# Performance work log

Measured on AMD Instinct MI355X. Metric: run time of the kernel, lower is better.

## Reference

```python
import jax, jax.numpy as jnp
import numpy as np
import math

B, L, C, Hh, Ww = 1, 16, 32, 64, 64
Wf = Ww // 2 + 1
R = 16
GROUPS = 4
MID = 4  # max(C//16, 4)
DT_REF = 1.0
INJ_K = 2.0
EPS = 1e-5


def _conv2d(x, w, b):
    y = jax.lax.conv_general_dilated(x, w, (1, 1), 'SAME',
                                     dimension_numbers=('NCHW', 'OIHW', 'NCHW'))
    return y + b[None, :, None, None]


def _adaptive_avg_w(x, out_w):
    # adaptive avg pool along last axis (torch AdaptiveAvgPool semantics)
    w_in = x.shape[-1]
    cs = jnp.concatenate([jnp.zeros(x.shape[:-1] + (1,), x.dtype), jnp.cumsum(x, -1)], -1)
    starts = np.floor(np.arange(out_w) * w_in / out_w).astype(np.int32)
    ends = np.ceil((np.arange(out_w) + 1) * w_in / out_w).astype(np.int32)
    num = cs[..., ends] - cs[..., starts]
    den = jnp.asarray(ends - starts, x.dtype)
    return num / den


def setup_inputs() -> dict:
    key = jax.random.key(0)
    ks = jax.random.split(key, 24)
    s = 0.05
    inp = {}
    inp['x'] = jax.random.normal(ks[0], (B, C, L, Hh, Ww), jnp.float32)
    inp['dt'] = jax.random.uniform(ks[1], (B, L), jnp.float32, 0.1, 1.0)
    inp['conv1_w'] = jax.random.normal(ks[2], (C, C, 3, 3), jnp.float32) * s
    inp['conv1_b'] = jnp.zeros((C,), jnp.float32)
    inp['conv2_w'] = jax.random.normal(ks[3], (C, C, 3, 3), jnp.float32) * s
    inp['conv2_b'] = jnp.zeros((C,), jnp.float32)
    inp['gfc_w'] = jax.random.normal(ks[4], (C, C), jnp.float32) * s
    inp['gfc_b'] = jnp.zeros((C,), jnp.float32)
    inp['head_w'] = jax.random.normal(ks[5], (C * R * 3, C), jnp.float32) * 0.02
    hb = np.zeros((C, R, 3), np.float32); hb[..., 0] = 1.0; hb[..., 2] = -5.0
    inp['head_b'] = jnp.asarray(hb.reshape(-1))
    inp['mix_w'] = jnp.eye(2 * R, dtype=jnp.float32) + jax.random.normal(ks[6], (2 * R, 2 * R), jnp.float32) * 0.02
    inp['mix_b'] = jnp.zeros((2 * R,), jnp.float32)
    inp['rank_scale'] = jnp.ones((R,), jnp.float32)
    inp['proj_w'] = jax.random.normal(ks[7], (1, R), jnp.float32) * s
    inp['proj_b'] = jnp.zeros((1,), jnp.float32)
    inp['pif_w'] = jax.random.normal(ks[8], (C, C), jnp.float32) * s  # 1x1x1 Conv3d
    inp['pif_b'] = jnp.zeros((C,), jnp.float32)
    inp['gn_w'] = jnp.ones((C,), jnp.float32)
    inp['gn_b'] = jnp.zeros((C,), jnp.float32)
    inp['g1_w'] = jax.random.normal(ks[9], (MID, C), jnp.float32) * s
    inp['g1_b'] = jnp.zeros((MID,), jnp.float32)
    inp['g2_w'] = jax.random.normal(ks[10], (C, MID), jnp.float32) * s
    inp['g2_b'] = jnp.zeros((C,), jnp.float32)
    return inp


def _forward(x, dt, conv1_w, conv1_b, conv2_w, conv2_b, gfc_w, gfc_b, head_w, head_b,
             mix_w, mix_b, rank_scale, proj_w, proj_b, pif_w, pif_b, gn_w, gn_b,
             g1_w, g1_b, g2_w, g2_b):
    Bx, Cx, Lx, H, W = x.shape
    x_seq = jnp.transpose(x, (0, 2, 1, 3, 4))  # [B,L,C,H,W]
    # ---- DynamicsParameterEstimator on flattened [B*L,C,H,W] ----
    xf = x_seq.reshape(Bx * Lx, Cx, H, W)
    f = jax.nn.silu(_conv2d(xf, conv1_w, conv1_b))
    f = jax.nn.silu(_conv2d(f, conv2_w, conv2_b))
    glob = jax.nn.sigmoid(f.mean((2, 3)) @ gfc_w.T + gfc_b)  # [BL,C]
    f = f * glob[:, :, None, None]
    f = _adaptive_avg_w(f.mean(2), Wf)         # [BL,C,Wf]
    feat = jnp.transpose(f, (0, 2, 1))          # [BL,Wf,C]
    p = (feat @ head_w.T + head_b).reshape(Bx * Lx, Wf, Cx, R, 3)
    nu = jax.nn.softplus(p[..., 0]).reshape(Bx, Lx, Wf, Cx, R)
    th = (jnp.tanh(p[..., 1]) * math.pi).reshape(Bx, Lx, Wf, Cx, R)
    sg = jax.nn.sigmoid(p[..., 2]).reshape(Bx, Lx, Wf, Cx, R)
    nu = jnp.transpose(nu, (0, 1, 3, 2, 4))[:, :, :, None]  # [B,L,C,1,Wf,R]
    th = jnp.transpose(th, (0, 1, 3, 2, 4))[:, :, :, None]
    sg = jnp.transpose(sg, (0, 1, 3, 2, 4))[:, :, :, None]
    # ---- Koopman A (triton kernel math): exp(-nu*dt) * exp(i*theta*dt) ----
    dtb = dt[:, :, None, None, None, None]
    decay = jnp.exp(-nu * dtb)
    ang = th * dtb
    A = jax.lax.complex(decay * jnp.cos(ang), decay * jnp.sin(ang))  # [B,L,C,1,Wf,R]
    # ---- injection in rfft space, gated by dt ----
    g = 1.0 - jnp.exp(-INJ_K * jnp.clip(dt / max(DT_REF, 1e-6), 0.0))  # [B,L]
    xfreq = jnp.fft.rfft(x_seq, axis=-1)        # [B,L,C,H,Wf] complex
    u = sg * xfreq[..., None] * g[:, :, None, None, None, None]  # [B,L,C,H,Wf,R]
    # ---- parallel linear recurrence h_t = A_t h_{t-1} + u_t ----
    def combine(a, b):
        Aa, ua = a
        Ab, ub = b
        return (Ab * Aa, Ab * ua + ub)
    _, h = jax.lax.associative_scan(combine, (A, u), axis=1)  # h: [B,L,C,H,Wf,R]
    # ---- SpectralMixer over rank (real/imag stacked) ----
    hs = jnp.concatenate([h.real, h.imag], -1) @ mix_w.T + mix_b
    hr, hi = jnp.split(hs, 2, -1)
    h = jax.lax.complex(hr, hi) * rank_scale
    # ---- rank projection + irfft ----
    y = jnp.einsum('blchfr,r->blchf', h, proj_w[0].astype(h.dtype)) + proj_b[0]
    y = jnp.fft.irfft(y, n=W, axis=-1)          # [B,L,C,H,W]
    y = jnp.transpose(y, (0, 2, 1, 3, 4))        # [B,C,L,H,W]
    # ---- post_ifft_proj: 1x1x1 Conv3d ----
    y = jnp.einsum('bclhw,oc->bolhw', y, pif_w) + pif_b[None, :, None, None, None]
    # ---- SpatialGroupNorm (per-frame GroupNorm, 4 groups) ----
    z = jnp.transpose(y, (0, 2, 1, 3, 4)).reshape(Bx * Lx, GROUPS, (Cx // GROUPS) * H * W)
    mu = z.mean(-1, keepdims=True)
    var = z.var(-1, keepdims=True)
    z = (z - mu) / jnp.sqrt(var + EPS)
    z = z.reshape(Bx, Lx, Cx, H, W) * gn_w[None, None, :, None, None] + gn_b[None, None, :, None, None]
    y = jnp.transpose(z, (0, 2, 1, 3, 4))        # [B,C,L,H,W]
    # ---- LatitudeGating (squeeze-excite over W) ----
    ym = y.mean(-1)                              # [B,C,L,H]
    yg = jnp.transpose(ym, (0, 2, 3, 1))          # [B,L,H,C]
    yg = jax.nn.sigmoid(jax.nn.silu(yg @ g1_w.T + g1_b) @ g2_w.T + g2_b)
    gate = jnp.transpose(yg, (0, 3, 1, 2))[..., None]  # [B,C,L,H,1]
    return x + y * gate


def reference(x, dt, conv1_w, conv1_b, conv2_w, conv2_b, gfc_w, gfc_b, head_w, head_b,
              mix_w, mix_b, rank_scale, proj_w, proj_b, pif_w, pif_b, gn_w, gn_b,
              g1_w, g1_b, g2_w, g2_b):
    return _forward(x, dt, conv1_w, conv1_b, conv2_w, conv2_b, gfc_w, gfc_b, head_w,
                    head_b, mix_w, mix_b, rank_scale, proj_w, proj_b, pif_w, pif_b,
                    gn_w, gn_b, g1_w, g1_b, g2_w, g2_b)
```

## Files before the change

### kernel.cpp

```cpp
#include <hip/hip_runtime.h>
#include <hip/hip_bf16.h>
#include <math.h>

#define CC 32
#define LL 16
#define HH 64
#define WW 64
#define WF 33
#define RR 16
#define PI_F 3.14159265358979323846f

typedef __attribute__((ext_vector_type(8))) short short8;
typedef __attribute__((ext_vector_type(4))) float f32x4;

#define OFF_F1      0
#define OFF_COLSUM  2097152
#define OFF_FEAT    2130944
#define OFF_ARE     2147840
#define OFF_AIM     2418176
#define OFF_SGG     2688512
#define OFF_XFR     2958848
#define OFF_XFI     4040192
#define OFF_YFR     5121536
#define OFF_YFI     6202880
#define OFF_PART    2958848
#define OFF_Y1      2958848
#define OFF_Y2      0
#define OFF_GNM     7284224
#define OFF_GNR     7284288
#define OFF_YM      7284352
#define OFF_GATE    7317120
#define OFF_WVEC    7349888
#define OFF_WT      7350016
#define OFF_YQ      7370496

__device__ __forceinline__ float sigmoidf_(float x){ return 1.0f/(1.0f+expf(-x)); }
__device__ __forceinline__ unsigned short f2bf(float v){
    __hip_bfloat16 b = __float2bfloat16(v);
    return *reinterpret_cast<unsigned short*>(&b);
}
__device__ __forceinline__ float bf2f(unsigned short u){
    __hip_bfloat16 b = *reinterpret_cast<__hip_bfloat16*>(&u);
    return __bfloat162float(b);
}

__global__ void k_prep0(const float* __restrict__ mix_w, const float* __restrict__ mix_b,
                        const float* __restrict__ rank_scale, const float* __restrict__ proj_w,
                        const float* __restrict__ proj_b,
                        const float* __restrict__ c1w, const float* __restrict__ c2w,
                        float* __restrict__ ws){
    unsigned short* wt = (unsigned short*)(ws + OFF_WT);
    if (blockIdx.x == 0){
        float* wv = ws + OFF_WVEC;
        int t = threadIdx.x;
        if (t < 32){
            float sre=0.f, sim=0.f;
            for (int r=0;r<RR;r++){
                float a = proj_w[r]*rank_scale[r];
                sre += a*mix_w[r*2*RR + t];
                sim += a*mix_w[(RR+r)*2*RR + t];
            }
            wv[t] = sre; wv[32+t] = sim;
        }
        if (t == 0){
            float cre=0.f, cim=0.f;
            for (int r=0;r<RR;r++){
                float a = proj_w[r]*rank_scale[r];
                cre += a*mix_b[r];
                cim += a*mix_b[RR+r];
            }
            wv[64] = cre + proj_b[0]; wv[65] = cim;
        }
        return;
    }
    int i = (blockIdx.x-1)*256 + threadIdx.x;
    if (i < 18432){
        int which = (i >= 9216);
        int j = which ? i - 9216 : i;
        int je   = j & 7;
        int lane = (j >> 3) & 63;
        int ct   = (j >> 9) & 1;
        int tap  = j >> 10;
        int kh = tap/3, kw = tap - kh*3;
        int co = ct*16 + (lane & 15);
        int ci = (lane >> 4)*8 + je;
        const float* cw = which ? c2w : c1w;
        wt[i] = f2bf(cw[((co*CC + ci)*3 + kh)*3 + kw]);
        return;
    }
    i -= 18432;
    if (i < 10240){
        int j = i & 7, lane = (i>>3)&63, cch = (i>>9)&3, t = i>>11;
        int frow = t*16 + (lane & 15);
        int k = ((lane>>4)&3)*8 + j;
        int w = (cch & 1)*32 + k;
        float coef = 0.f;
        if (frow < 33)       coef =  cosf(2.0f*PI_F*(float)(frow*w)/64.0f);
        else if (frow < 66)  coef = -sinf(2.0f*PI_F*(float)((frow-33)*w)/64.0f);
        unsigned short hi = f2bf(coef);
        wt[18432 + i] = (cch < 2) ? hi : f2bf(coef - bf2f(hi));
        return;
    }
    i -= 10240;
    if (i < 12288){
        int wtile = i / 3072;
        int rem = i - wtile*3072;
        int ch = rem >> 9;
        int ll = rem & 511;
        int lane = ll >> 3, j = ll & 7;
        int w = wtile*16 + (lane & 15);
        int k = (ch % 3)*32 + ((lane>>4)&3)*8 + j;
        float coef = 0.f;
        if (k < 33){
            float s = (k==0 || k==32) ? 1.f : 2.f;
            coef = s*cosf(2.0f*PI_F*(float)(k*w)/64.0f)*(1.0f/64.0f);
        } else if (k < 66){
            int f = k - 33;
            float s = (f==0 || f==32) ? 1.f : 2.f;
            coef = -s*sinf(2.0f*PI_F*(float)(f*w)/64.0f)*(1.0f/64.0f);
        }
        unsigned short hi = f2bf(coef);
        wt[18432 + 10240 + i] = (ch < 3) ? hi : f2bf(coef - bf2f(hi));
        return;
    }
}

__global__ __launch_bounds__(256, 4) void k_conv1m(const float* __restrict__ x,
                                                   const unsigned short* __restrict__ wt,
                                                   const float* __restrict__ cb,
                                                   unsigned short* __restrict__ f1p){
    __shared__ __align__(16) unsigned short xs[4*66*32];
    __shared__ __align__(16) unsigned short pw[9216];

    const int tid  = threadIdx.x;
    const int l    = blockIdx.x >> 5;
    const int h0   = (blockIdx.x & 31)*2;
    const int wid  = tid >> 6;
    const int lane = tid & 63;
    const int col  = lane & 15;
    const int kgrp = lane >> 4;

    {
        const unsigned int* src = (const unsigned int*)wt;
        unsigned int* dst = (unsigned int*)pw;
        #pragma unroll
        for (int j = 0; j < 18; ++j) dst[tid + j*256] = src[tid + j*256];
    }
    {
        const int rr = tid >> 6;
        const int w  = tid & 63;
        int hh = h0 - 1 + rr;
        bool hv = (hh >= 0 && hh < HH);
        const float* sp = x + (long)l*HH*WW + hh*WW + w;
        int wIdx = 1 + w;
        #pragma unroll
        for (int cib = 0; cib < 4; ++cib){
            float v[8];
            #pragma unroll
            for (int k = 0; k < 8; ++k)
                v[k] = hv ? sp[(long)(cib*8 + k)*LL*HH*WW] : 0.f;
            uint4 p;
            p.x = (unsigned)f2bf(v[0]) | ((unsigned)f2bf(v[1])<<16);
            p.y = (unsigned)f2bf(v[2]) | ((unsigned)f2bf(v[3])<<16);
            p.z = (unsigned)f2bf(v[4]) | ((unsigned)f2bf(v[5])<<16);
            p.w = (unsigned)f2bf(v[6]) | ((unsigned)f2bf(v[7])<<16);
            int cs = cib ^ (wIdx & 3);
            *(uint4*)&xs[(rr*66 + wIdx)*32 + cs*8] = p;
        }
    }
    if (tid < 32){
        int row = tid >> 3, rest = tid & 7;
        int wIdx = (rest >> 2) ? 65 : 0;
        int cib = rest & 3;
        *(uint4*)&xs[(row*66 + wIdx)*32 + cib*8] = make_uint4(0,0,0,0);
    }
    __syncthreads();

    #pragma unroll
    for (int u = 0; u < 4; ++u){
        int unit = wid + u*4;
        int hloc = unit >> 3;
        int rem  = unit & 7;
        int ct   = rem >> 2;
        int wt16 = rem & 3;
        int colw = wt16*16 + col;
        f32x4 acc = {0.f,0.f,0.f,0.f};
        #pragma unroll
        for (int kh = 0; kh < 3; ++kh){
            #pragma unroll
            for (int kw = 0; kw < 3; ++kw){
                int wIdx = colw + kw;
                int cs = kgrp ^ (wIdx & 3);
                short8 b = *(const short8*)&xs[((hloc+kh)*66 + wIdx)*32 + cs*8];
                short8 a = *(const short8*)&pw[((kh*3+kw)*2 + ct)*512 + lane*8];
                acc = __builtin_amdgcn_mfma_f32_16x16x32_bf16(a, b, acc, 0, 0, 0);
            }
        }
        int co0 = ct*16 + kgrp*4;
        int h = h0 + hloc;
        float o[4];
        #pragma unroll
        for (int r = 0; r < 4; ++r){
            float v = acc[r] + cb[co0+r];
            o[r] = v * sigmoidf_(v);
        }
        uint2 pk;
        pk.x = (unsigned)f2bf(o[0]) | ((unsigned)f2bf(o[1])<<16);
        pk.y = (unsigned)f2bf(o[2]) | ((unsigned)f2bf(o[3])<<16);
        *(uint2*)&f1p[(((long)l*HH + h)*WW + colw)*32 + co0] = pk;
    }
}

__global__ __launch_bounds__(256, 4) void k_conv2m(const unsigned short* __restrict__ f1p,
                                                   const unsigned short* __restrict__ wt,
                                                   const float* __restrict__ cb,
                                                   float* __restrict__ ws){
    __shared__ __align__(16) unsigned short xs[4*66*32];
    __shared__ __align__(16) unsigned short pw[9216];

    const int tid  = threadIdx.x;
    const int l    = blockIdx.x >> 5;
    const int h0   = (blockIdx.x & 31)*2;
    const int wid  = tid >> 6;
    const int lane = tid & 63;
    const int col  = lane & 15;
    const int kgrp = lane >> 4;

    {
        const unsigned int* src = (const unsigned int*)wt;
        unsigned int* dst = (unsigned int*)pw;
        #pragma unroll
        for (int j = 0; j < 18; ++j) dst[tid + j*256] = src[tid + j*256];
    }
    {
        const int rr = tid >> 6;
        const int w  = tid & 63;
        int hh = h0 - 1 + rr;
        bool hv = (hh >= 0 && hh < HH);
        const uint4* sp = (const uint4*)&f1p[(((long)l*HH + hh)*WW + w)*32];
        int wIdx = 1 + w;
        #pragma unroll
        for (int cib = 0; cib < 4; ++cib){
            uint4 p = hv ? sp[cib] : make_uint4(0,0,0,0);
            int cs = cib ^ (wIdx & 3);
            *(uint4*)&xs[(rr*66 + wIdx)*32 + cs*8] = p;
        }
    }
    if (tid < 32){
        int row = tid >> 3, rest = tid & 7;
        int wIdx = (rest >> 2) ? 65 : 0;
        int cib = rest & 3;
        *(uint4*)&xs[(row*66 + wIdx)*32 + cib*8] = make_uint4(0,0,0,0);
    }
    __syncthreads();

    #pragma unroll
    for (int u = 0; u < 4; ++u){
        int unit = wid + u*4;
        int hloc = unit >> 3;
        int rem  = unit & 7;
        int ct   = rem >> 2;
        int wt16 = rem & 3;
        int colw = wt16*16 + col;
        f32x4 acc = {0.f,0.f,0.f,0.f};
        #pragma unroll
        for (int kh = 0; kh < 3; ++kh){
            #pragma unroll
            for (int kw = 0; kw < 3; ++kw){
                int wIdx = colw + kw;
                int cs = kgrp ^ (wIdx & 3);
                short8 b = *(const short8*)&xs[((hloc+kh)*66 + wIdx)*32 + cs*8];
                short8 a = *(const short8*)&pw[((kh*3+kw)*2 + ct)*512 + lane*8];
                acc = __builtin_amdgcn_mfma_f32_16x16x32_bf16(a, b, acc, 0, 0, 0);
            }
        }
        int co0 = ct*16 + kgrp*4;
        int h = h0 + hloc;
        float* pp = ws + OFF_PART + ((long)(l*HH + h))*2048 + colw;
        #pragma unroll
        for (int r = 0; r < 4; ++r){
            float v = acc[r] + cb[co0+r];
            pp[(co0+r)*WW] = v * sigmoidf_(v);
        }
    }
}

__global__ void k_colred(float* __restrict__ ws){
    int b = blockIdx.x;
    int l = b >> 5, c = b & 31;
    int w = threadIdx.x;
    const float* p = ws + OFF_PART + (long)l*HH*2048 + c*WW + w;
    float s = 0.f;
    #pragma unroll 8
    for (int h = 0; h < HH; ++h) s += p[h*2048];
    ws[OFF_COLSUM + (l*CC + c)*WW + w] = s;
}

__global__ void k_globfeat(const float* __restrict__ gfc_w, const float* __restrict__ gfc_b,
                           float* __restrict__ ws){
    __shared__ float gs[CC], gl[CC];
    int l = blockIdx.x;
    int tid = threadIdx.x;
    if (tid < 32){
        const float* cs = ws + OFF_COLSUM + (l*CC+tid)*WW;
        float s = 0.f;
        for (int w=0;w<WW;w++) s += cs[w];
        gs[tid] = s;
    }
    __syncthreads();
    if (tid < 32){
        float acc = gfc_b[tid];
        for (int i=0;i<CC;i++) acc += gs[i]*(1.0f/4096.0f)*gfc_w[tid*CC+i];
        gl[tid] = sigmoidf_(acc);
    }
    __syncthreads();
    for (int i = tid; i < WF*CC; i += 256){
        int c = i & 31, wf = i >> 5;
        int s = (wf*64)/33;
        int e = ((wf+1)*64 + 32)/33;
        const float* cs = ws + OFF_COLSUM + (l*CC+c)*WW;
        float sum = 0.f;
        for (int w=s;w<e;w++) sum += cs[w];
        ws[OFF_FEAT + (l*WF+wf)*CC + c] = gl[c] * sum / (64.0f*(float)(e-s));
    }
}

__global__ void k_head(const float* __restrict__ hw, const float* __restrict__ hb,
                       const float* __restrict__ dt, float* __restrict__ ws){
    int t = blockIdx.x*blockDim.x + threadIdx.x;
    if (t >= LL*WF*CC*RR) return;
    int r = t & 15, c = (t>>4) & 31;
    int lw_ = t >> 9;
    int wf = lw_ % WF, l = lw_ / WF;
    const float* feat = ws + OFF_FEAT + (l*WF+wf)*CC;
    int j0 = (c*RR + r)*3;
    const float* w0 = hw + j0*CC;
    float p0=hb[j0], p1=hb[j0+1], p2=hb[j0+2];
    for (int i=0;i<CC;i++){
        float fv = feat[i];
        p0 += fv*w0[i]; p1 += fv*w0[CC+i]; p2 += fv*w0[2*CC+i];
    }
    float nu = fmaxf(p0,0.f) + log1pf(expf(-fabsf(p0)));
    float th = tanhf(p1)*PI_F;
    float sg = sigmoidf_(p2);
    float dtv = dt[l];
    float decay = expf(-nu*dtv);
    float ang = th*dtv;
    float g = 1.0f - expf(-2.0f*fmaxf(dtv,0.f));
    int idx = ((l*CC+c)*WF+wf)*RR + r;
    ws[OFF_ARE+idx] = decay*cosf(ang);
    ws[OFF_AIM+idx] = decay*sinf(ang);
    ws[OFF_SGG+idx] = sg*g;
}

__global__ __launch_bounds__(256, 4) void k_rfftm(const float* __restrict__ x,
                                                  const unsigned short* __restrict__ at,
                                                  float* __restrict__ ws){
    __shared__ __align__(16) unsigned short xs[HH*68];
    int b = blockIdx.x; int l = b >> 5, c = b & 31;
    int tid = threadIdx.x;
    const int wid  = tid >> 6;
    const int lane = tid & 63;
    const int col  = lane & 15;
    const int kgrp = lane >> 4;

    const float* xp = x + (long)(c*LL + l)*HH*WW;
    for (int i = tid; i < HH*WW; i += 256){
        int h = i >> 6, w = i & 63;
        xs[h*68 + w] = f2bf(xp[i]);
    }
    __syncthreads();

    float* xfr = ws + OFF_XFR + (long)(l*CC + c)*HH*WF;
    float* xfi = ws + OFF_XFI + (long)(l*CC + c)*HH*WF;
    #pragma unroll
    for (int q = 0; q < 5; ++q){
        int unit = wid + q*4;
        int ftile = unit >> 2;
        int htile = unit & 3;
        f32x4 acc = {0.f,0.f,0.f,0.f};
        #pragma unroll
        for (int cch = 0; cch < 4; ++cch){
            short8 a = *(const short8*)&at[(((ftile*4 + cch)*64) + lane)*8];
            short8 bb = *(const short8*)&xs[(htile*16 + col)*68 + (cch & 1)*32 + kgrp*8];
            acc = __builtin_amdgcn_mfma_f32_16x16x32_bf16(a, bb, acc, 0, 0, 0);
        }
        int h = htile*16 + col;
        #pragma unroll
        for (int r = 0; r < 4; ++r){
            int fr = ftile*16 + kgrp*4 + r;
            if (fr < 33)      xfr[fr*HH + h] = acc[r];
            else if (fr < 66) xfi[(fr-33)*HH + h] = acc[r];
        }
    }
}

__global__ __launch_bounds__(256) void k_scan(float* __restrict__ ws){
    __shared__ float lA[LL*RR], lI[LL*RR], lS[LL*RR];
    __shared__ float wv[66];
    int b = blockIdx.x;
    int c = b / WF, f = b - c*WF;
    int tid = threadIdx.x;
    if (tid < 66) wv[tid] = ws[OFF_WVEC + tid];
    {
        int l = tid >> 4, r = tid & 15;
        int src = ((l*CC + c)*WF + f)*RR + r;
        lA[tid] = ws[OFF_ARE + src];
        lI[tid] = ws[OFF_AIM + src];
        lS[tid] = ws[OFF_SGG + src];
    }
    __syncthreads();
    const int h  = tid >> 2;
    const int rq = tid & 3;
    float sre[4] = {0,0,0,0}, sim[4] = {0,0,0,0};
    float w0_[4], w1_[4], w2_[4], w3_[4];
    #pragma unroll
    for (int q=0;q<4;q++){
        int r = rq*4 + q;
        w0_[q]=wv[r]; w1_[q]=wv[16+r]; w2_[q]=wv[32+r]; w3_[q]=wv[48+r];
    }
    const float cre = wv[64], cim = wv[65];
    const long fh = (long)(c*WF + f)*HH + h;
    #pragma unroll 1
    for (int l=0;l<LL;l++){
        float xr = ws[OFF_XFR + l*(CC*HH*WF) + fh];
        float xi = ws[OFF_XFI + l*(CC*HH*WF) + fh];
        float yr = 0.f, yi = 0.f;
        #pragma unroll
        for (int q=0;q<4;q++){
            int r = rq*4 + q;
            float a = lA[l*16+r], ii = lI[l*16+r], s = lS[l*16+r];
            float nre = a*sre[q] - ii*sim[q] + s*xr;
            float nim = a*sim[q] + ii*sre[q] + s*xi;
            sre[q]=nre; sim[q]=nim;
            yr += w0_[q]*nre + w1_[q]*nim;
            yi += w2_[q]*nre + w3_[q]*nim;
        }
        yr += __shfl_xor(yr, 1); yr += __shfl_xor(yr, 2);
        yi += __shfl_xor(yi, 1); yi += __shfl_xor(yi, 2);
        if (rq == 0){
            ws[OFF_YFR + l*(CC*HH*WF) + fh] = yr + cre;
            ws[OFF_YFI + l*(CC*HH*WF) + fh] = yi + cim;
        }
    }
}

__global__ __launch_bounds__(256, 4) void k_irfftm(const unsigned short* __restrict__ btb,
                                                   float* __restrict__ ws){
    __shared__ __align__(16) unsigned short mh[HH*100];
    int b = blockIdx.x; int l = b >> 5, c = b & 31;
    int tid = threadIdx.x;
    const int wid  = tid >> 6;
    const int lane = tid & 63;
    const int col  = lane & 15;
    const int kgrp = lane >> 4;

    const float* Yr = ws + OFF_YFR + (long)(l*CC + c)*HH*WF;
    const float* Yi = ws + OFF_YFI + (long)(l*CC + c)*HH*WF;
    for (int i = tid; i < 33*64; i += 256){
        int f = i >> 6, h = i & 63;
        mh[h*100 + f]      = f2bf(Yr[i]);
        mh[h*100 + 33 + f] = f2bf(Yi[i]);
    }
    for (int i = tid; i < 64*34; i += 256){
        int h = i / 34, f = 66 + (i - (i/34)*34);
        mh[h*100 + f] = 0;
    }
    __syncthreads();

    float* y1 = ws + OFF_Y1 + (long)(l*CC + c)*HH*WW;
    #pragma unroll
    for (int q = 0; q < 4; ++q){
        int unit = wid + q*4;
        int htile = unit >> 2;
        int wtile = unit & 3;
        f32x4 acc = {0.f,0.f,0.f,0.f};
        #pragma unroll
        for (int ch = 0; ch < 6; ++ch){
            int kof = (ch % 3)*32 + kgrp*8;
            short8 a = *(const short8*)&mh[(htile*16 + col)*100 + kof];
            short8 bb = *(const short8*)&btb[(((wtile*6 + ch)*64) + lane)*8];
            acc = __builtin_amdgcn_mfma_f32_16x16x32_bf16(a, bb, acc, 0, 0, 0);
        }
        int w = wtile*16 + col;
        #pragma unroll
        for (int r = 0; r < 4; ++r){
            int h = htile*16 + kgrp*4 + r;
            y1[h*WW + w] = acc[r];
        }
    }
}

__global__ void k_pif(const float* __restrict__ pw, const float* __restrict__ pb,
                      float* __restrict__ ws){
    __shared__ float row[CC][WW];
    int b = blockIdx.x; int l = b>>6, h = b&63;
    int tid = threadIdx.x;
    for (int k=0;k<8;k++){
        int i = tid + k*256;
        int ci = i>>6, w = i&63;
        row[ci][w] = ws[OFF_Y1 + ((l*CC+ci)*HH + h)*WW + w];
    }
    __syncthreads();
    for (int k=0;k<8;k++){
        int i = tid + k*256;
        int o = i>>6, w = i&63;
        float acc = pb[o];
        #pragma unroll
        for (int ci=0;ci<CC;ci++) acc += pw[o*CC+ci]*row[ci][w];
        ws[OFF_Y2 + ((l*CC+o)*HH + h)*WW + w] = acc;
        float s = acc, q = acc*acc;
        s += __shfl_down(s, 32, 64); q += __shfl_down(q, 32, 64);
        s += __shfl_down(s, 16, 64); q += __shfl_down(q, 16, 64);
        s += __shfl_down(s,  8, 64); q += __shfl_down(q,  8, 64);
        s += __shfl_down(s,  4, 64); q += __shfl_down(q,  4, 64);
        s += __shfl_down(s,  2, 64); q += __shfl_down(q,  2, 64);
        s += __shfl_down(s,  1, 64); q += __shfl_down(q,  1, 64);
        if ((tid & 63) == 0){
            ws[OFF_YM + (l*HH+h)*CC + o] = s*(1.0f/64.0f);
            ws[OFF_YQ + (l*HH+h)*CC + o] = q;
        }
    }
}

__global__ void k_gnred(float* __restrict__ ws){
    __shared__ float rs[256], rq[256];
    int b = blockIdx.x; int l = b>>2, g = b&3;
    int tid = threadIdx.x;
    float s=0.f, q=0.f;
    for (int j = tid; j < 512; j += 256){
        int h = j >> 3, cc = j & 7;
        int off = (l*HH+h)*CC + g*8 + cc;
        s += ws[OFF_YM + off];
        q += ws[OFF_YQ + off];
    }
    rs[tid]=s; rq[tid]=q; __syncthreads();
    for (int off=128; off>0; off>>=1){
        if (tid<off){ rs[tid]+=rs[tid+off]; rq[tid]+=rq[tid+off]; }
        __syncthreads();
    }
    if (tid==0){
        float mean = rs[0]*(1.0f/512.0f);
        float ex2  = rq[0]*(1.0f/32768.0f);
        float var = ex2 - mean*mean;
        ws[OFF_GNM + b] = mean;
        ws[OFF_GNR + b] = rsqrtf(var + 1e-5f);
    }
}

__global__ void k_gate(const float* __restrict__ g1w, const float* __restrict__ g1b,
                       const float* __restrict__ g2w, const float* __restrict__ g2b,
                       const float* __restrict__ gnw, const float* __restrict__ gnb,
                       float* __restrict__ ws){
    int t = blockIdx.x*256 + threadIdx.x;
    if (t >= LL*HH*CC) return;
    int c = t & 31, h = (t>>5)&63, l = t>>11;
    const float* ym = ws + OFF_YM + (l*HH+h)*CC;
    float mus[4], rsd[4];
    #pragma unroll
    for (int g=0; g<4; ++g){ mus[g] = ws[OFF_GNM + l*4+g]; rsd[g] = ws[OFF_GNR + l*4+g]; }
    float ymn[CC];
    #pragma unroll
    for (int i=0;i<CC;i++){
        int g = i>>3;
        ymn[i] = (ym[i] - mus[g])*rsd[g]*gnw[i] + gnb[i];
    }
    float mid[4];
    #pragma unroll
    for (int m=0;m<4;m++){
        float a = g1b[m];
        #pragma unroll
        for (int i=0;i<CC;i++) a += ymn[i]*g1w[m*CC+i];
        mid[m] = a*sigmoidf_(a);
    }
    float a = g2b[c];
    #pragma unroll
    for (int m=0;m<4;m++) a += mid[m]*g2w[c*4+m];
    ws[OFF_GATE + t] = sigmoidf_(a);
}

__global__ void k_final(const float* __restrict__ x, float* __restrict__ out,
                        const float* __restrict__ gnw, const float* __restrict__ gnb,
                        const float* __restrict__ ws){
    int t = blockIdx.x*256 + threadIdx.x;
    int n = t*4;
    int h = (n>>6)&63, l = (n>>12)&15, c = n>>16;
    int g = c>>3;
    float mu = ws[OFF_GNM + l*4+g], rstd = ws[OFF_GNR + l*4+g];
    float gw = gnw[c]*rstd, gb = gnb[c] - mu*gnw[c]*rstd;
    float4 z  = *(const float4*)(ws + OFF_Y2 + (((l*CC+c)*HH+h)*WW) + (n&63));
    float  gt = ws[OFF_GATE + (l*HH+h)*CC + c];
    float4 xv = *(const float4*)(x + n);
    float4 o;
    o.x = xv.x + (z.x*gw+gb)*gt; o.y = xv.y + (z.y*gw+gb)*gt;
    o.z = xv.z + (z.z*gw+gb)*gt; o.w = xv.w + (z.w*gw+gb)*gt;
    *(float4*)(out + n) = o;
}

extern "C" void kernel_launch(void* const* d_in, const int* in_sizes, int n_in,
                              void* d_out, int out_size, void* d_ws, size_t ws_size,
                              hipStream_t stream){
    const float* x    = (const float*)d_in[0];
    const float* dt   = (const float*)d_in[1];
    const float* c1w  = (const float*)d_in[2];
    const float* c1b  = (const float*)d_in[3];
    const float* c2w  = (const float*)d_in[4];
    const float* c2b  = (const float*)d_in[5];
    const float* gfcw = (const float*)d_in[6];
    const float* gfcb = (const float*)d_in[7];
    const float* hw   = (const float*)d_in[8];
    const float* hb   = (const float*)d_in[9];
    const float* mixw = (const float*)d_in[10];
    const float* mixb = (const float*)d_in[11];
    const float* rs   = (const float*)d_in[12];
    const float* pjw  = (const float*)d_in[13];
    const float* pjb  = (const float*)d_in[14];
    const float* pifw = (const float*)d_in[15];
    const float* pifb = (const float*)d_in[16];
    const float* gnw  = (const float*)d_in[17];
    const float* gnb  = (const float*)d_in[18];
    const float* g1w  = (const float*)d_in[19];
    const float* g1b  = (const float*)d_in[20];
    const float* g2w  = (const float*)d_in[21];
    const float* g2b  = (const float*)d_in[22];
    float* ws  = (float*)d_ws;
    float* out = (float*)d_out;
    unsigned short* wt  = (unsigned short*)(ws + OFF_WT);
    unsigned short* at  = wt + 18432;
    unsigned short* btb = wt + 18432 + 10240;
    unsigned short* f1p = (unsigned short*)(ws + OFF_F1);

    k_prep0   <<<161,  256, 0, stream>>>(mixw, mixb, rs, pjw, pjb, c1w, c2w, ws);
    k_conv1m  <<<512,  256, 0, stream>>>(x, wt, c1b, f1p);
    k_conv2m  <<<512,  256, 0, stream>>>(f1p, wt + 9216, c2b, ws);
    k_colred  <<<512,  64,  0, stream>>>(ws);
    k_globfeat<<<16,   256, 0, stream>>>(gfcw, gfcb, ws);
    k_head    <<<1056, 256, 0, stream>>>(hw, hb, dt, ws);
    k_rfftm   <<<512,  256, 0, stream>>>(x, at, ws);
    k_scan    <<<1056, 256, 0, stream>>>(ws);
    k_irfftm  <<<512,  256, 0, stream>>>(btb, ws);
    k_pif     <<<1024, 256, 0, stream>>>(pifw, pifb, ws);
    k_gnred   <<<64,   256, 0, stream>>>(ws);
    k_gate    <<<128,  256, 0, stream>>>(g1w, g1b, g2w, g2b, gnw, gnb, ws);
    k_final   <<<2048, 256, 0, stream>>>(x, out, gnw, gnb, ws);
}
```

Before: 208.2 us.

## Fuse head projection into scan and merge GroupNorm reduction with gate

The per-(l,c,wf,r) head projection and its transcendental decay/angle math now run inside k_scan, which computes them into shared memory instead of reading them from global arrays written by a separate kernel. The GroupNorm statistics reduction and the latitude gate MLP are merged into one kernel that reduces group stats per block with wave shuffles and computes the gate for a 16-row slab. This removes two kernel launches and the global round trips for the A/S coefficients and GN stats. In exchange, each scan block recomputes the head projection for its channel/frequency, and every gate block redundantly recomputes the full GN reduction.

```diff
diff --git a/kernel.cpp b/kernel.cpp
--- a/kernel.cpp
+++ b/kernel.cpp
@@ -16,9 +16,6 @@
 #define OFF_F1      0
 #define OFF_COLSUM  2097152
 #define OFF_FEAT    2130944
-#define OFF_ARE     2147840
-#define OFF_AIM     2418176
-#define OFF_SGG     2688512
 #define OFF_XFR     2958848
 #define OFF_XFI     4040192
 #define OFF_YFR     5121536
@@ -325,34 +322,6 @@
     }
 }
 
-__global__ void k_head(const float* __restrict__ hw, const float* __restrict__ hb,
-                       const float* __restrict__ dt, float* __restrict__ ws){
-    int t = blockIdx.x*blockDim.x + threadIdx.x;
-    if (t >= LL*WF*CC*RR) return;
-    int r = t & 15, c = (t>>4) & 31;
-    int lw_ = t >> 9;
-    int wf = lw_ % WF, l = lw_ / WF;
-    const float* feat = ws + OFF_FEAT + (l*WF+wf)*CC;
-    int j0 = (c*RR + r)*3;
-    const float* w0 = hw + j0*CC;
-    float p0=hb[j0], p1=hb[j0+1], p2=hb[j0+2];
-    for (int i=0;i<CC;i++){
-        float fv = feat[i];
-        p0 += fv*w0[i]; p1 += fv*w0[CC+i]; p2 += fv*w0[2*CC+i];
-    }
-    float nu = fmaxf(p0,0.f) + log1pf(expf(-fabsf(p0)));
-    float th = tanhf(p1)*PI_F;
-    float sg = sigmoidf_(p2);
-    float dtv = dt[l];
-    float decay = expf(-nu*dtv);
-    float ang = th*dtv;
-    float g = 1.0f - expf(-2.0f*fmaxf(dtv,0.f));
-    int idx = ((l*CC+c)*WF+wf)*RR + r;
-    ws[OFF_ARE+idx] = decay*cosf(ang);
-    ws[OFF_AIM+idx] = decay*sinf(ang);
-    ws[OFF_SGG+idx] = sg*g;
-}
-
 __global__ __launch_bounds__(256, 4) void k_rfftm(const float* __restrict__ x,
                                                   const unsigned short* __restrict__ at,
                                                   float* __restrict__ ws){
@@ -395,19 +364,42 @@
     }
 }
 
-__global__ __launch_bounds__(256) void k_scan(float* __restrict__ ws){
+__global__ __launch_bounds__(256) void k_scan(const float* __restrict__ hw,
+                                              const float* __restrict__ hb,
+                                              const float* __restrict__ dt,
+                                              float* __restrict__ ws){
     __shared__ float lA[LL*RR], lI[LL*RR], lS[LL*RR];
     __shared__ float wv[66];
+    __shared__ float lfeat[LL*CC];
     int b = blockIdx.x;
     int c = b / WF, f = b - c*WF;
     int tid = threadIdx.x;
     if (tid < 66) wv[tid] = ws[OFF_WVEC + tid];
+    for (int i = tid; i < LL*CC; i += 256){
+        int l = i >> 5, ii = i & 31;
+        lfeat[i] = ws[OFF_FEAT + (l*WF + f)*CC + ii];
+    }
+    __syncthreads();
     {
         int l = tid >> 4, r = tid & 15;
-        int src = ((l*CC + c)*WF + f)*RR + r;
-        lA[tid] = ws[OFF_ARE + src];
-        lI[tid] = ws[OFF_AIM + src];
-        lS[tid] = ws[OFF_SGG + src];
+        const float* feat = lfeat + l*CC;
+        int j0 = (c*RR + r)*3;
+        const float* w0 = hw + j0*CC;
+        float p0=hb[j0], p1=hb[j0+1], p2=hb[j0+2];
+        #pragma unroll 8
+        for (int i=0;i<CC;i++){
+            float fv = feat[i];
+            p0 += fv*w0[i]; p1 += fv*w0[CC+i]; p2 += fv*w0[2*CC+i];
+        }
+        float nu = fmaxf(p0,0.f) + log1pf(expf(-fabsf(p0)));
+        float th = tanhf(p1)*PI_F;
+        float sg = sigmoidf_(p2);
+        float dtv = dt[l];
+        float decay = expf(-nu*dtv);
+        float ang = th*dtv;
+        lA[tid] = decay*cosf(ang);
+        lI[tid] = decay*sinf(ang);
+        lS[tid] = sg*(1.0f - expf(-2.0f*fmaxf(dtv,0.f)));
     }
     __syncthreads();
     const int h  = tid >> 2;
@@ -523,60 +515,59 @@
     }
 }
 
-__global__ void k_gnred(float* __restrict__ ws){
-    __shared__ float rs[256], rq[256];
-    int b = blockIdx.x; int l = b>>2, g = b&3;
+__global__ void k_gatel(const float* __restrict__ g1w, const float* __restrict__ g1b,
+                        const float* __restrict__ g2w, const float* __restrict__ g2b,
+                        const float* __restrict__ gnw, const float* __restrict__ gnb,
+                        float* __restrict__ ws){
+    __shared__ float mus[4], rsd[4];
+    __shared__ float ymn[16][CC+1];
+    __shared__ float mid[16][4];
+    int blk = blockIdx.x;
+    int l = blk >> 2, hq = blk & 3;
+    int h0 = hq*16;
     int tid = threadIdx.x;
-    float s=0.f, q=0.f;
-    for (int j = tid; j < 512; j += 256){
-        int h = j >> 3, cc = j & 7;
-        int off = (l*HH+h)*CC + g*8 + cc;
-        s += ws[OFF_YM + off];
-        q += ws[OFF_YQ + off];
-    }
-    rs[tid]=s; rq[tid]=q; __syncthreads();
-    for (int off=128; off>0; off>>=1){
-        if (tid<off){ rs[tid]+=rs[tid+off]; rq[tid]+=rq[tid+off]; }
-        __syncthreads();
-    }
-    if (tid==0){
-        float mean = rs[0]*(1.0f/512.0f);
-        float ex2  = rq[0]*(1.0f/32768.0f);
-        float var = ex2 - mean*mean;
-        ws[OFF_GNM + b] = mean;
-        ws[OFF_GNR + b] = rsqrtf(var + 1e-5f);
-    }
-}
-
-__global__ void k_gate(const float* __restrict__ g1w, const float* __restrict__ g1b,
-                       const float* __restrict__ g2w, const float* __restrict__ g2b,
-                       const float* __restrict__ gnw, const float* __restrict__ gnb,
-                       float* __restrict__ ws){
-    int t = blockIdx.x*256 + threadIdx.x;
-    if (t >= LL*HH*CC) return;
-    int c = t & 31, h = (t>>5)&63, l = t>>11;
-    const float* ym = ws + OFF_YM + (l*HH+h)*CC;
-    float mus[4], rsd[4];
-    #pragma unroll
-    for (int g=0; g<4; ++g){ mus[g] = ws[OFF_GNM + l*4+g]; rsd[g] = ws[OFF_GNR + l*4+g]; }
-    float ymn[CC];
-    #pragma unroll
-    for (int i=0;i<CC;i++){
-        int g = i>>3;
-        ymn[i] = (ym[i] - mus[g])*rsd[g]*gnw[i] + gnb[i];
-    }
-    float mid[4];
-    #pragma unroll
-    for (int m=0;m<4;m++){
+
+    {
+        int g = tid >> 6, j = tid & 63;
+        const float* ymp = ws + OFF_YM + (l*HH + j)*CC + g*8;
+        const float* yqp = ws + OFF_YQ + (l*HH + j)*CC + g*8;
+        float s = 0.f, q = 0.f;
+        #pragma unroll
+        for (int cc = 0; cc < 8; ++cc){ s += ymp[cc]; q += yqp[cc]; }
+        #pragma unroll
+        for (int off = 32; off > 0; off >>= 1){
+            s += __shfl_down(s, off, 64);
+            q += __shfl_down(q, off, 64);
+        }
+        if (j == 0){
+            float mean = s*(1.0f/512.0f);
+            float rstd = rsqrtf(q*(1.0f/32768.0f) - mean*mean + 1e-5f);
+            mus[g] = mean; rsd[g] = rstd;
+            if (hq == 0){ ws[OFF_GNM + l*4+g] = mean; ws[OFF_GNR + l*4+g] = rstd; }
+        }
+    }
+    __syncthreads();
+    for (int i = tid; i < 16*CC; i += 256){
+        int hh = i >> 5, cidx = i & 31;
+        int g = cidx >> 3;
+        ymn[hh][cidx] = (ws[OFF_YM + (l*HH + h0 + hh)*CC + cidx] - mus[g])*rsd[g]*gnw[cidx] + gnb[cidx];
+    }
+    __syncthreads();
+    if (tid < 64){
+        int hh = tid >> 2, m = tid & 3;
         float a = g1b[m];
-        #pragma unroll
-        for (int i=0;i<CC;i++) a += ymn[i]*g1w[m*CC+i];
-        mid[m] = a*sigmoidf_(a);
-    }
-    float a = g2b[c];
-    #pragma unroll
-    for (int m=0;m<4;m++) a += mid[m]*g2w[c*4+m];
-    ws[OFF_GATE + t] = sigmoidf_(a);
+        #pragma unroll 8
+        for (int i = 0; i < CC; ++i) a += ymn[hh][i]*g1w[m*CC+i];
+        mid[hh][m] = a*sigmoidf_(a);
+    }
+    __syncthreads();
+    for (int i = tid; i < 16*CC; i += 256){
+        int hh = i >> 5, cidx = i & 31;
+        float a = g2b[cidx];
+        #pragma unroll
+        for (int m = 0; m < 4; ++m) a += mid[hh][m]*g2w[cidx*4+m];
+        ws[OFF_GATE + (l*HH + h0 + hh)*CC + cidx] = sigmoidf_(a);
+    }
 }
 
 __global__ void k_final(const float* __restrict__ x, float* __restrict__ out,
@@ -635,12 +626,10 @@
     k_conv2m  <<<512,  256, 0, stream>>>(f1p, wt + 9216, c2b, ws);
     k_colred  <<<512,  64,  0, stream>>>(ws);
     k_globfeat<<<16,   256, 0, stream>>>(gfcw, gfcb, ws);
-    k_head    <<<1056, 256, 0, stream>>>(hw, hb, dt, ws);
     k_rfftm   <<<512,  256, 0, stream>>>(x, at, ws);
-    k_scan    <<<1056, 256, 0, stream>>>(ws);
+    k_scan    <<<1056, 256, 0, stream>>>(hw, hb, dt, ws);
     k_irfftm  <<<512,  256, 0, stream>>>(btb, ws);
     k_pif     <<<1024, 256, 0, stream>>>(pifw, pifb, ws);
-    k_gnred   <<<64,   256, 0, stream>>>(ws);
-    k_gate    <<<128,  256, 0, stream>>>(g1w, g1b, g2w, g2b, gnw, gnb, ws);
+    k_gatel   <<<64,   256, 0, stream>>>(g1w, g1b, g2w, g2b, gnw, gnb, ws);
     k_final   <<<2048, 256, 0, stream>>>(x, out, gnw, gnb, ws);
 }
```

Measured after the change: 201.4 us. 1.03x faster.
